# Kernel tuning notes

Measured on AMD Instinct MI355X. Metric: run time of the kernel, lower is better.

## Reference

```python
import jax, jax.numpy as jnp
import numpy as np

N_NODES = 100000
N_EDGES = 1600000
D_IN = 128
D_HID = 64
D_EMB = 64
EDGE_DIM = 2 * D_EMB  # 128
N_CASES = 4
BATCH = 16384
BN_EPS = 1e-5


def gcn_conv(x, src, dst, n, W, b):
    # PyG GCNConv: linear transform, add self-loops, sym-normalized aggregation
    h = x @ W  # [N, out]
    loop = jnp.arange(n, dtype=src.dtype)
    s = jnp.concatenate([src, loop])
    d = jnp.concatenate([dst, loop])
    deg = jax.ops.segment_sum(jnp.ones(s.shape[0], dtype=h.dtype), d, num_segments=n)
    dinv = jnp.where(deg > 0, deg ** -0.5, 0.0)
    norm = dinv[s] * dinv[d]  # [E+N]
    msg = h[s] * norm[:, None]
    return jax.ops.segment_sum(msg, d, num_segments=n) + b


def batchnorm(h, gamma, beta):
    # BatchNorm1d in training mode: biased batch statistics over nodes
    mu = h.mean(0)
    var = jnp.mean((h - mu) ** 2, axis=0)
    return (h - mu) * jax.lax.rsqrt(var + BN_EPS) * gamma + beta


def gcn_net(x, src, dst, n, W1, b1, g, be, W2, b2):
    h = gcn_conv(x, src, dst, n, W1, b1)
    h = jax.nn.relu(batchnorm(h, g, be))
    return gcn_conv(h, src, dst, n, W2, b2)


def setup_inputs() -> dict:
    key = jax.random.key(0)
    ks = jax.random.split(key, 20)
    inp = {
        "x": jax.random.normal(ks[0], (N_NODES, D_IN), dtype=jnp.float32),
        "edge_index": jax.random.randint(ks[1], (2, N_EDGES), 0, N_NODES, dtype=jnp.int32),
        "users_tensor": jax.random.randint(ks[2], (BATCH,), 0, 50000, dtype=jnp.int64) if jax.config.jax_enable_x64 else jax.random.randint(ks[2], (BATCH,), 0, 50000, dtype=jnp.int32),
        "items_tensor": jax.random.randint(ks[3], (BATCH,), 0, N_NODES, dtype=jnp.int32),
    }
    s = 0.05
    # generalized GCN params
    inp["W1g"] = jax.random.normal(ks[4], (D_IN, D_HID), dtype=jnp.float32) * s
    inp["b1g"] = jnp.zeros((D_HID,), jnp.float32)
    inp["g1g"] = jnp.ones((D_HID,), jnp.float32)
    inp["be1g"] = jnp.zeros((D_HID,), jnp.float32)
    inp["W2g"] = jax.random.normal(ks[5], (D_HID, D_EMB), dtype=jnp.float32) * s
    inp["b2g"] = jnp.zeros((D_EMB,), jnp.float32)
    # specific GCN params
    inp["W1s"] = jax.random.normal(ks[6], (D_IN, D_HID), dtype=jnp.float32) * s
    inp["b1s"] = jnp.zeros((D_HID,), jnp.float32)
    inp["g1s"] = jnp.ones((D_HID,), jnp.float32)
    inp["be1s"] = jnp.zeros((D_HID,), jnp.float32)
    inp["W2s"] = jax.random.normal(ks[7], (D_HID, D_EMB), dtype=jnp.float32) * s
    inp["b2s"] = jnp.zeros((D_EMB,), jnp.float32)
    # fusion gate (note: original forward uses hidden1 for BOTH inputs)
    inp["Wf1"] = jax.random.normal(ks[8], (EDGE_DIM, EDGE_DIM), dtype=jnp.float32) * s
    inp["Wsig"] = jax.random.normal(ks[9], (2 * EDGE_DIM, 1), dtype=jnp.float32) * s
    # heads
    inp["Wtc"] = jax.random.normal(ks[10], (EDGE_DIM, N_CASES), dtype=jnp.float32) * s
    inp["btc"] = jnp.zeros((N_CASES,), jnp.float32)
    inp["Wp"] = jax.random.normal(ks[11], (EDGE_DIM, 2), dtype=jnp.float32) * s
    inp["bp"] = jnp.zeros((2,), jnp.float32)
    return inp


def reference(x, edge_index, users_tensor, items_tensor,
              W1g, b1g, g1g, be1g, W2g, b2g,
              W1s, b1s, g1s, be1s, W2s, b2s,
              Wf1, Wsig, Wtc, btc, Wp, bp):
    n = x.shape[0]
    src, dst = edge_index[0], edge_index[1]

    nodes_gen = gcn_net(x, src, dst, n, W1g, b1g, g1g, be1g, W2g, b2g)  # [N, D_EMB]
    nodes_spec = gcn_net(x, src, dst, n, W1s, b1s, g1s, be1s, W2s, b2s)

    gen = jnp.concatenate([nodes_gen[users_tensor], nodes_gen[items_tensor]], axis=1)   # [B, 2E]
    spec = jnp.concatenate([nodes_spec[users_tensor], nodes_spec[items_tensor]], axis=1)

    h1 = jnp.tanh(gen @ Wf1)
    h2 = jnp.tanh(spec @ Wf1)  # original reuses hidden1
    z = jax.nn.sigmoid(jnp.concatenate([h1, h2], axis=1) @ Wsig)  # [B,1]
    fused = z * h1 + (1.0 - z) * h2

    link_output = fused @ Wp + bp
    generalized_output = gen @ Wtc + btc
    return (link_output, generalized_output)
```

## Files before the change

### kernel.cpp

```cpp
#include <hip/hip_runtime.h>
#include <hip/hip_bf16.h>


#define ELL_CAP 64
#define BCAP 8192
#define ACHUNK 5120

typedef __attribute__((ext_vector_type(8))) short short8v;
typedef __attribute__((ext_vector_type(4))) float f32x4;

static __device__ __forceinline__ float wred64(float v) {
#pragma unroll
  for (int m = 32; m; m >>= 1) v += __shfl_xor(v, m, 64);
  return v;
}

static __device__ __forceinline__ unsigned short f2bf(float f) {
  unsigned u = __float_as_uint(f);
  unsigned r = (u + 0x7fffu + ((u >> 16) & 1u)) >> 16;
  return (unsigned short)r;
}
static __device__ __forceinline__ unsigned packbf(float a, float b) {
  return (unsigned)f2bf(a) | ((unsigned)f2bf(b) << 16);
}
static __device__ __forceinline__ float bflo(unsigned u) {
  return __uint_as_float(u << 16);
}
static __device__ __forceinline__ float bfhi(unsigned u) {
  return __uint_as_float(u & 0xffff0000u);
}

__global__ void k_prep(const float* __restrict__ x, unsigned* __restrict__ bff,
                       int* __restrict__ gbump, float* __restrict__ stats,
                       const float* __restrict__ W1g, const float* __restrict__ b1g,
                       const float* __restrict__ W1s, const float* __restrict__ b1s,
                       const float* __restrict__ W2g, const float* __restrict__ b2g,
                       const float* __restrict__ W2s, const float* __restrict__ b2s,
                       const float* __restrict__ Wf1,
                       short* __restrict__ Wb1, short* __restrict__ Wb2,
                       short* __restrict__ WbH, float* __restrict__ bc1,
                       float* __restrict__ bc2, int n, int NB) {
  int idx = blockIdx.x * 256 + threadIdx.x;
  int n16 = n * 16;
  if (idx < n16) {
    const float4* f4 = (const float4*)x;
    float4 a = f4[idx * 2], b = f4[idx * 2 + 1];
    uint4 o;
    o.x = packbf(a.x, a.y);
    o.y = packbf(a.z, a.w);
    o.z = packbf(b.x, b.y);
    o.w = packbf(b.z, b.w);
    ((uint4*)bff)[idx] = o;
  }
  if (idx < 16384) {
    int k = idx >> 7, c = idx & 127;
    int pi = (k >> 3) * 1024 + c * 8 + (k & 7);
    float w1 = (c < 64) ? W1g[k * 64 + c] : W1s[k * 64 + (c - 64)];
    Wb1[pi] = (short)f2bf(w1);
    float w2 = 0.f;
    if (k < 64 && c < 64) w2 = W2g[k * 64 + c];
    else if (k >= 64 && c >= 64) w2 = W2s[(k - 64) * 64 + (c - 64)];
    Wb2[pi] = (short)f2bf(w2);
    WbH[pi] = (short)f2bf(Wf1[k * 128 + c]);
  }
  if (idx < 128) {
    bc1[idx] = (idx < 64) ? b1g[idx] : b1s[idx - 64];
    bc2[idx] = (idx < 64) ? b2g[idx] : b2s[idx - 64];
  }
  if (idx < NB) gbump[idx] = idx * BCAP;
  if (idx < 2048) stats[idx] = 0.f;
}

__global__ __launch_bounds__(256) void k_bucketA(
    const int* __restrict__ src, const int* __restrict__ dst,
    int* __restrict__ gbump, unsigned* __restrict__ ebuf, int E, int NB) {
  __shared__ int hist[512];
  __shared__ int gbase[512];
  int t = threadIdx.x;
  int e0 = blockIdx.x * ACHUNK;
  int m = min(ACHUNK, E - e0);
  for (int b = t; b < NB; b += 256) hist[b] = 0;
  __syncthreads();
  for (int i = t; i < m; i += 256) atomicAdd(&hist[dst[e0 + i] >> 8], 1);
  __syncthreads();
  for (int b = t; b < NB; b += 256) {
    gbase[b] = hist[b] ? atomicAdd(&gbump[b], hist[b]) : 0;
    hist[b] = 0;
  }
  __syncthreads();
  for (int i = t; i < m; i += 256) {
    int d = dst[e0 + i];
    int s = src[e0 + i];
    int b = d >> 8;
    int off = gbase[b] + atomicAdd(&hist[b], 1);
    if (off < (b + 1) * BCAP)
      ebuf[off] = ((unsigned)s << 8) | (unsigned)(d & 255);
  }
}

__global__ __launch_bounds__(256) void k_csrB(
    const unsigned* __restrict__ ebuf, const int* __restrict__ gbump,
    int* __restrict__ cnt, float* __restrict__ dinv, int* __restrict__ col,
    int n) {
  __shared__ int lbump[256];
  int b = blockIdx.x;
  lbump[threadIdx.x] = 0;
  __syncthreads();
  int base = b * BCAP;
  int m = min(gbump[b] - base, BCAP);
  for (int i = threadIdx.x; i < m; i += 256) {
    unsigned p = ebuf[base + i];
    int dloc = p & 255;
    int slot = atomicAdd(&lbump[dloc], 1);
    if (slot < ELL_CAP)
      col[(b * 256 + dloc) * ELL_CAP + slot] = (int)(p >> 8);
  }
  __syncthreads();
  int node = b * 256 + threadIdx.x;
  if (node < n) {
    int c = lbump[threadIdx.x];
    cnt[node] = min(c, ELL_CAP);
    dinv[node] = rsqrtf((float)(c + 1));
  }
}

template <bool BN>
__global__ __launch_bounds__(256) void k_agg(
    const unsigned* __restrict__ featb, unsigned* __restrict__ outb,
    const int* __restrict__ cnt, const float* __restrict__ dinv,
    const int* __restrict__ col,
    const float* __restrict__ stats, const float* __restrict__ g1g,
    const float* __restrict__ be1g, const float* __restrict__ g1s,
    const float* __restrict__ be1s, float inv_n, int n) {
  __shared__ float sc_sh[128], sf_sh[128];
  if (BN) {
    int c = threadIdx.x;
    if (c < 128) {
      float s = 0.f, q = 0.f;
#pragma unroll
      for (int k = 0; k < 8; k++) {
        s += stats[k * 256 + c];
        q += stats[k * 256 + 128 + c];
      }
      float mu = s * inv_n;
      float var = q * inv_n - mu * mu;
      float gam = (c < 64) ? g1g[c] : g1s[c - 64];
      float bet = (c < 64) ? be1g[c] : be1s[c - 64];
      float scv = gam * rsqrtf(var + 1e-5f);
      sc_sh[c] = scv;
      sf_sh[c] = bet - mu * scv;
    }
    __syncthreads();
  }
  int node = blockIdx.x * 16 + (threadIdx.x >> 4);
  if (node >= n) return;
  int t = threadIdx.x & 15;
  float sc[8], sf[8];
  if (BN) {
#pragma unroll
    for (int j = 0; j < 8; j++) {
      sc[j] = sc_sh[8 * t + j];
      sf[j] = sf_sh[8 * t + j];
    }
  }
  const uint4* f4 = (const uint4*)featb;
  float di = dinv[node];
  float acc[8];
  {
    uint4 sv = f4[node * 16 + t];
    float f[8] = {bflo(sv.x), bfhi(sv.x), bflo(sv.y), bfhi(sv.y),
                  bflo(sv.z), bfhi(sv.z), bflo(sv.w), bfhi(sv.w)};
#pragma unroll
    for (int j = 0; j < 8; j++) {
      if (BN) f[j] = fmaxf(f[j] * sc[j] + sf[j], 0.f);
      acc[j] = f[j] * di;
    }
  }
  int m = cnt[node];
  const int4* cl = (const int4*)&col[node * ELL_CAP];
  int i = 0;
  for (; i + 8 <= m; i += 8) {
    int4 c0 = cl[i >> 2];
    int4 c1 = cl[(i >> 2) + 1];
    int ss[8] = {c0.x, c0.y, c0.z, c0.w, c1.x, c1.y, c1.z, c1.w};
    float ww[8];
    uint4 vv[8];
#pragma unroll
    for (int q = 0; q < 8; q++) {
      ww[q] = dinv[ss[q]];
      vv[q] = f4[ss[q] * 16 + t];
    }
#pragma unroll
    for (int q = 0; q < 8; q++) {
      float w = ww[q];
      uint4 v = vv[q];
      float f[8] = {bflo(v.x), bfhi(v.x), bflo(v.y), bfhi(v.y),
                    bflo(v.z), bfhi(v.z), bflo(v.w), bfhi(v.w)};
#pragma unroll
      for (int j = 0; j < 8; j++) {
        if (BN) f[j] = fmaxf(f[j] * sc[j] + sf[j], 0.f);
        acc[j] += f[j] * w;
      }
    }
  }
  for (; i + 4 <= m; i += 4) {
    int4 c4 = cl[i >> 2];
    int ss[4] = {c4.x, c4.y, c4.z, c4.w};
#pragma unroll
    for (int q = 0; q < 4; q++) {
      int s = ss[q];
      float w = dinv[s];
      uint4 v = f4[s * 16 + t];
      float f[8] = {bflo(v.x), bfhi(v.x), bflo(v.y), bfhi(v.y),
                    bflo(v.z), bfhi(v.z), bflo(v.w), bfhi(v.w)};
#pragma unroll
      for (int j = 0; j < 8; j++) {
        if (BN) f[j] = fmaxf(f[j] * sc[j] + sf[j], 0.f);
        acc[j] += f[j] * w;
      }
    }
  }
  for (; i < m; ++i) {
    int s = col[node * ELL_CAP + i];
    float w = dinv[s];
    uint4 v = f4[s * 16 + t];
    float f[8] = {bflo(v.x), bfhi(v.x), bflo(v.y), bfhi(v.y),
                  bflo(v.z), bfhi(v.z), bflo(v.w), bfhi(v.w)};
#pragma unroll
    for (int j = 0; j < 8; j++) {
      if (BN) f[j] = fmaxf(f[j] * sc[j] + sf[j], 0.f);
      acc[j] += f[j] * w;
    }
  }
  uint4 o;
  o.x = packbf(acc[0] * di, acc[1] * di);
  o.y = packbf(acc[2] * di, acc[3] * di);
  o.z = packbf(acc[4] * di, acc[5] * di);
  o.w = packbf(acc[6] * di, acc[7] * di);
  ((uint4*)outb)[node * 16 + t] = o;
}

template <bool CBF16, bool STATS, bool TANH, bool GATHER>
__global__ __launch_bounds__(256) void k_mgemm(
    const unsigned* __restrict__ Abf, const unsigned short* __restrict__ nodesb,
    const int* __restrict__ users, const int* __restrict__ items,
    const short* __restrict__ Wb, const float* __restrict__ bias,
    void* __restrict__ Cvp, int M, float* __restrict__ stats) {
  __shared__ short Wl[16384];
  __shared__ float shs[128], shq[128];
  {
    const uint4* s4 = (const uint4*)Wb;
    uint4* d4 = (uint4*)Wl;
    for (int i = threadIdx.x; i < 2048; i += 256) d4[i] = s4[i];
  }
  if (STATS && threadIdx.x < 128) { shs[threadIdx.x] = 0.f; shq[threadIdx.x] = 0.f; }
  __syncthreads();
  int lane = threadIdx.x & 63;
  int wv = threadIdx.x >> 6;
  int l15 = lane & 15;
  int l4 = lane >> 4;
  int row = blockIdx.x * 64 + wv * 16 + l15;
  int rc = min(row, M - 1);
  bool valid = row < M;

  short8v afr[4];
  if (GATHER) {
    int fo = blockIdx.y * 64;
    const short* pu = (const short*)nodesb + users[rc] * 128 + fo;
    const short* pi = (const short*)nodesb + items[rc] * 128 + fo;
#pragma unroll
    for (int ks = 0; ks < 4; ks++) {
      int k = ks * 32 + l4 * 8;
      const short* p = (ks < 2) ? (pu + k) : (pi + (k - 64));
      afr[ks] = *(const short8v*)p;
    }
  } else {
    const short* Ab = (const short*)Abf + (size_t)rc * 128;
#pragma unroll
    for (int ks = 0; ks < 4; ks++)
      afr[ks] = *(const short8v*)(Ab + ks * 32 + l4 * 8);
  }

  f32x4 acc[8];
#pragma unroll
  for (int nt = 0; nt < 8; nt++) acc[nt] = (f32x4){0.f, 0.f, 0.f, 0.f};
#pragma unroll
  for (int nt = 0; nt < 8; nt++) {
#pragma unroll
    for (int ks = 0; ks < 4; ks++) {
      int kb = ks * 4 + l4;
      short8v w = *(const short8v*)&Wl[kb * 1024 + (nt * 16 + l15) * 8];
      acc[nt] = __builtin_amdgcn_mfma_f32_16x16x32_bf16(w, afr[ks], acc[nt], 0, 0, 0);
    }
  }

#pragma unroll
  for (int nt = 0; nt < 8; nt++) {
    int c0 = nt * 16 + l4 * 4;
    float o[4];
#pragma unroll
    for (int r = 0; r < 4; r++) o[r] = acc[nt][r];
    if (bias) {
      float4 bv = *(const float4*)(bias + c0);
      o[0] += bv.x; o[1] += bv.y; o[2] += bv.z; o[3] += bv.w;
    }
    if (TANH) {
#pragma unroll
      for (int r = 0; r < 4; r++) o[r] = tanhf(o[r]);
    }
    if (STATS) {
      float s[4], q[4];
#pragma unroll
      for (int r = 0; r < 4; r++) {
        s[r] = valid ? o[r] : 0.f;
        q[r] = s[r] * s[r];
      }
#pragma unroll
      for (int m = 1; m < 16; m <<= 1) {
#pragma unroll
        for (int r = 0; r < 4; r++) {
          s[r] += __shfl_xor(s[r], m, 64);
          q[r] += __shfl_xor(q[r], m, 64);
        }
      }
      if (l15 == 0) {
#pragma unroll
        for (int r = 0; r < 4; r++) {
          atomicAdd(&shs[c0 + r], s[r]);
          atomicAdd(&shq[c0 + r], q[r]);
        }
      }
    }
    if (valid) {
      if (CBF16) {
        unsigned* Cb = (unsigned*)Cvp;
        uint2 p;
        p.x = packbf(o[0], o[1]);
        p.y = packbf(o[2], o[3]);
        *(uint2*)&Cb[(size_t)row * 64 + (c0 >> 1)] = p;
      } else {
        float* Cf = (float*)Cvp + (size_t)blockIdx.y * M * 128;
        *(float4*)&Cf[(size_t)row * 128 + c0] = make_float4(o[0], o[1], o[2], o[3]);
      }
    }
  }
  if (STATS) {
    __syncthreads();
    if (threadIdx.x < 128) {
      float* st = stats + (blockIdx.x & 7) * 256;
      atomicAdd(&st[threadIdx.x], shs[threadIdx.x]);
      atomicAdd(&st[128 + threadIdx.x], shq[threadIdx.x]);
    }
  }
}

__global__ void k_head(const float* __restrict__ G1, const float* __restrict__ G2,
                       const unsigned short* __restrict__ nodesb,
                       const int* __restrict__ users,
                       const int* __restrict__ items, const float* __restrict__ Wsig,
                       const float* __restrict__ Wtc, const float* __restrict__ btc,
                       const float* __restrict__ Wp, const float* __restrict__ bp,
                       float* __restrict__ out, int B) {
  int l = threadIdx.x & 63;
  int wave = (blockIdx.x * 256 + threadIdx.x) >> 6;
  int nw = (gridDim.x * 256) >> 6;
  for (int b = wave; b < B; b += nw) {
    const float* g1 = G1 + (size_t)b * 128;
    const float* g2 = G2 + (size_t)b * 128;
    int u = users[b], it = items[b];
    float h1a = g1[l], h1b = g1[64 + l];
    float h2a = g2[l], h2b = g2[64 + l];
    float ga = __uint_as_float((unsigned)nodesb[u * 128 + l] << 16);
    float gb = __uint_as_float((unsigned)nodesb[it * 128 + l] << 16);
    float zp = h1a * Wsig[l] + h1b * Wsig[64 + l] + h2a * Wsig[128 + l] + h2b * Wsig[192 + l];
    float z = wred64(zp);
    z = 1.f / (1.f + expf(-z));
    float fa = z * h1a + (1.f - z) * h2a;
    float fb = z * h1b + (1.f - z) * h2b;
    float p0 = wred64(fa * Wp[l * 2] + fb * Wp[(64 + l) * 2]);
    float p1 = wred64(fa * Wp[l * 2 + 1] + fb * Wp[(64 + l) * 2 + 1]);
    float t0 = wred64(ga * Wtc[l * 4] + gb * Wtc[(64 + l) * 4]);
    float t1 = wred64(ga * Wtc[l * 4 + 1] + gb * Wtc[(64 + l) * 4 + 1]);
    float t2 = wred64(ga * Wtc[l * 4 + 2] + gb * Wtc[(64 + l) * 4 + 2]);
    float t3 = wred64(ga * Wtc[l * 4 + 3] + gb * Wtc[(64 + l) * 4 + 3]);
    if (l == 0) {
      out[b * 2] = p0 + bp[0];
      out[b * 2 + 1] = p1 + bp[1];
      float* go = out + 2 * B;
      go[b * 4] = t0 + btc[0];
      go[b * 4 + 1] = t1 + btc[1];
      go[b * 4 + 2] = t2 + btc[2];
      go[b * 4 + 3] = t3 + btc[3];
    }
  }
}

extern "C" void kernel_launch(void* const* d_in, const int* in_sizes, int n_in,
                              void* d_out, int out_size, void* d_ws, size_t ws_size,
                              hipStream_t stream) {
  const float* x = (const float*)d_in[0];
  const int* ei = (const int*)d_in[1];
  const int* users = (const int*)d_in[2];
  const int* items = (const int*)d_in[3];
  const float* W1g = (const float*)d_in[4];
  const float* b1g = (const float*)d_in[5];
  const float* g1g = (const float*)d_in[6];
  const float* be1g = (const float*)d_in[7];
  const float* W2g = (const float*)d_in[8];
  const float* b2g = (const float*)d_in[9];
  const float* W1s = (const float*)d_in[10];
  const float* b1s = (const float*)d_in[11];
  const float* g1s = (const float*)d_in[12];
  const float* be1s = (const float*)d_in[13];
  const float* W2s = (const float*)d_in[14];
  const float* b2s = (const float*)d_in[15];
  const float* Wf1 = (const float*)d_in[16];
  const float* Wsig = (const float*)d_in[17];
  const float* Wtc = (const float*)d_in[18];
  const float* btc = (const float*)d_in[19];
  const float* Wp = (const float*)d_in[20];
  const float* bp = (const float*)d_in[21];

  int n = in_sizes[0] / 128;
  int E = in_sizes[1] / 2;
  int B = in_sizes[2];
  int NB = (n + 255) >> 8;
  const int* srcp = ei;
  const int* dstp = ei + E;
  float* out = (float*)d_out;

  char* w = (char*)d_ws;
  auto alloc = [&](size_t bytes) -> char* {
    char* p = w;
    w += (bytes + 255) & ~(size_t)255;
    return p;
  };
  unsigned* xab = (unsigned*)alloc((size_t)n * 64 * 4);
  float* big1 = (float*)alloc((size_t)n * 128 * 4);
  unsigned* bff = (unsigned*)alloc((size_t)n * 128 * 2);
  int* col = (int*)alloc((size_t)n * ELL_CAP * 4);
  unsigned* ebuf = (unsigned*)alloc((size_t)NB * BCAP * 4);
  int* cnt = (int*)alloc((size_t)n * 4);
  float* dinv = (float*)alloc((size_t)n * 4);
  int* gbump = (int*)alloc(512 * 4);
  short* Wb1 = (short*)alloc(16384 * 2);
  short* Wb2 = (short*)alloc(16384 * 2);
  short* WbH = (short*)alloc(16384 * 2);
  float* bc1 = (float*)alloc(512);
  float* bc2 = (float*)alloc(512);
  float* stats = (float*)alloc(2048 * 4);

  k_prep<<<(n * 16 + 255) / 256, 256, 0, stream>>>(
      x, bff, gbump, stats, W1g, b1g, W1s, b1s, W2g, b2g, W2s, b2s, Wf1,
      Wb1, Wb2, WbH, bc1, bc2, n, NB);
  k_bucketA<<<(E + ACHUNK - 1) / ACHUNK, 256, 0, stream>>>(srcp, dstp, gbump, ebuf, E, NB);
  k_csrB<<<NB, 256, 0, stream>>>(ebuf, gbump, cnt, dinv, col, n);

  unsigned* hb = (unsigned*)big1;
  unsigned short* nodesb = (unsigned short*)big1;

  k_agg<false><<<(n + 15) / 16, 256, 0, stream>>>(bff, xab, cnt, dinv, col,
                                                  nullptr, nullptr, nullptr,
                                                  nullptr, nullptr, 0.f, n);
  k_mgemm<true, true, false, false><<<(n + 63) / 64, 256, 0, stream>>>(
      xab, nullptr, nullptr, nullptr, Wb1, bc1, hb, n, stats);

  k_agg<true><<<(n + 15) / 16, 256, 0, stream>>>(hb, xab, cnt, dinv, col,
                                                 stats, g1g, be1g, g1s, be1s,
                                                 1.f / (float)n, n);
  k_mgemm<true, false, false, false><<<(n + 63) / 64, 256, 0, stream>>>(
      xab, nullptr, nullptr, nullptr, Wb2, bc2, nodesb, n, nullptr);

  float* G1 = (float*)bff;
  dim3 gh((B + 63) / 64, 2);
  k_mgemm<false, false, true, true><<<gh, 256, 0, stream>>>(
      nullptr, nodesb, users, items, WbH, nullptr, G1, B, nullptr);
  float* G2 = G1 + (size_t)B * 128;
  k_head<<<2048, 256, 0, stream>>>(G1, G2, nodesb, users, items, Wsig, Wtc, btc,
                                   Wp, bp, out, B);
}
```

Before: 275.8 us.

## Fuse head GEMM and link head into one MFMA kernel; drop 8-wide agg unroll

Result: faster. 250.5 us (-9.2%).

```diff
diff --git a/kernel.cpp b/kernel.cpp
--- a/kernel.cpp
+++ b/kernel.cpp
@@ -8,12 +8,6 @@
 
 typedef __attribute__((ext_vector_type(8))) short short8v;
 typedef __attribute__((ext_vector_type(4))) float f32x4;
-
-static __device__ __forceinline__ float wred64(float v) {
-#pragma unroll
-  for (int m = 32; m; m >>= 1) v += __shfl_xor(v, m, 64);
-  return v;
-}
 
 static __device__ __forceinline__ unsigned short f2bf(float f) {
   unsigned u = __float_as_uint(f);
@@ -28,6 +22,9 @@
 }
 static __device__ __forceinline__ float bfhi(unsigned u) {
   return __uint_as_float(u & 0xffff0000u);
+}
+static __device__ __forceinline__ float bf2f(short s) {
+  return __uint_as_float((unsigned)(unsigned short)s << 16);
 }
 
 __global__ void k_prep(const float* __restrict__ x, unsigned* __restrict__ bff,
@@ -179,30 +176,6 @@
   int m = cnt[node];
   const int4* cl = (const int4*)&col[node * ELL_CAP];
   int i = 0;
-  for (; i + 8 <= m; i += 8) {
-    int4 c0 = cl[i >> 2];
-    int4 c1 = cl[(i >> 2) + 1];
-    int ss[8] = {c0.x, c0.y, c0.z, c0.w, c1.x, c1.y, c1.z, c1.w};
-    float ww[8];
-    uint4 vv[8];
-#pragma unroll
-    for (int q = 0; q < 8; q++) {
-      ww[q] = dinv[ss[q]];
-      vv[q] = f4[ss[q] * 16 + t];
-    }
-#pragma unroll
-    for (int q = 0; q < 8; q++) {
-      float w = ww[q];
-      uint4 v = vv[q];
-      float f[8] = {bflo(v.x), bfhi(v.x), bflo(v.y), bfhi(v.y),
-                    bflo(v.z), bfhi(v.z), bflo(v.w), bfhi(v.w)};
-#pragma unroll
-      for (int j = 0; j < 8; j++) {
-        if (BN) f[j] = fmaxf(f[j] * sc[j] + sf[j], 0.f);
-        acc[j] += f[j] * w;
-      }
-    }
-  }
   for (; i + 4 <= m; i += 4) {
     int4 c4 = cl[i >> 2];
     int ss[4] = {c4.x, c4.y, c4.z, c4.w};
@@ -240,10 +213,9 @@
   ((uint4*)outb)[node * 16 + t] = o;
 }
 
-template <bool CBF16, bool STATS, bool TANH, bool GATHER>
+template <bool CBF16, bool STATS>
 __global__ __launch_bounds__(256) void k_mgemm(
-    const unsigned* __restrict__ Abf, const unsigned short* __restrict__ nodesb,
-    const int* __restrict__ users, const int* __restrict__ items,
+    const unsigned* __restrict__ Abf,
     const short* __restrict__ Wb, const float* __restrict__ bias,
     void* __restrict__ Cvp, int M, float* __restrict__ stats) {
   __shared__ short Wl[16384];
@@ -264,22 +236,10 @@
   bool valid = row < M;
 
   short8v afr[4];
-  if (GATHER) {
-    int fo = blockIdx.y * 64;
-    const short* pu = (const short*)nodesb + users[rc] * 128 + fo;
-    const short* pi = (const short*)nodesb + items[rc] * 128 + fo;
-#pragma unroll
-    for (int ks = 0; ks < 4; ks++) {
-      int k = ks * 32 + l4 * 8;
-      const short* p = (ks < 2) ? (pu + k) : (pi + (k - 64));
-      afr[ks] = *(const short8v*)p;
-    }
-  } else {
-    const short* Ab = (const short*)Abf + (size_t)rc * 128;
-#pragma unroll
-    for (int ks = 0; ks < 4; ks++)
-      afr[ks] = *(const short8v*)(Ab + ks * 32 + l4 * 8);
-  }
+  const short* Ab = (const short*)Abf + (size_t)rc * 128;
+#pragma unroll
+  for (int ks = 0; ks < 4; ks++)
+    afr[ks] = *(const short8v*)(Ab + ks * 32 + l4 * 8);
 
   f32x4 acc[8];
 #pragma unroll
@@ -303,10 +263,6 @@
     if (bias) {
       float4 bv = *(const float4*)(bias + c0);
       o[0] += bv.x; o[1] += bv.y; o[2] += bv.z; o[3] += bv.w;
-    }
-    if (TANH) {
-#pragma unroll
-      for (int r = 0; r < 4; r++) o[r] = tanhf(o[r]);
     }
     if (STATS) {
       float s[4], q[4];
@@ -339,7 +295,7 @@
         p.y = packbf(o[2], o[3]);
         *(uint2*)&Cb[(size_t)row * 64 + (c0 >> 1)] = p;
       } else {
-        float* Cf = (float*)Cvp + (size_t)blockIdx.y * M * 128;
+        float* Cf = (float*)Cvp;
         *(float4*)&Cf[(size_t)row * 128 + c0] = make_float4(o[0], o[1], o[2], o[3]);
       }
     }
@@ -354,44 +310,120 @@
   }
 }
 
-__global__ void k_head(const float* __restrict__ G1, const float* __restrict__ G2,
-                       const unsigned short* __restrict__ nodesb,
-                       const int* __restrict__ users,
-                       const int* __restrict__ items, const float* __restrict__ Wsig,
-                       const float* __restrict__ Wtc, const float* __restrict__ btc,
-                       const float* __restrict__ Wp, const float* __restrict__ bp,
-                       float* __restrict__ out, int B) {
-  int l = threadIdx.x & 63;
-  int wave = (blockIdx.x * 256 + threadIdx.x) >> 6;
-  int nw = (gridDim.x * 256) >> 6;
-  for (int b = wave; b < B; b += nw) {
-    const float* g1 = G1 + (size_t)b * 128;
-    const float* g2 = G2 + (size_t)b * 128;
-    int u = users[b], it = items[b];
-    float h1a = g1[l], h1b = g1[64 + l];
-    float h2a = g2[l], h2b = g2[64 + l];
-    float ga = __uint_as_float((unsigned)nodesb[u * 128 + l] << 16);
-    float gb = __uint_as_float((unsigned)nodesb[it * 128 + l] << 16);
-    float zp = h1a * Wsig[l] + h1b * Wsig[64 + l] + h2a * Wsig[128 + l] + h2b * Wsig[192 + l];
-    float z = wred64(zp);
-    z = 1.f / (1.f + expf(-z));
-    float fa = z * h1a + (1.f - z) * h2a;
-    float fb = z * h1b + (1.f - z) * h2b;
-    float p0 = wred64(fa * Wp[l * 2] + fb * Wp[(64 + l) * 2]);
-    float p1 = wred64(fa * Wp[l * 2 + 1] + fb * Wp[(64 + l) * 2 + 1]);
-    float t0 = wred64(ga * Wtc[l * 4] + gb * Wtc[(64 + l) * 4]);
-    float t1 = wred64(ga * Wtc[l * 4 + 1] + gb * Wtc[(64 + l) * 4 + 1]);
-    float t2 = wred64(ga * Wtc[l * 4 + 2] + gb * Wtc[(64 + l) * 4 + 2]);
-    float t3 = wred64(ga * Wtc[l * 4 + 3] + gb * Wtc[(64 + l) * 4 + 3]);
-    if (l == 0) {
-      out[b * 2] = p0 + bp[0];
-      out[b * 2 + 1] = p1 + bp[1];
-      float* go = out + 2 * B;
-      go[b * 4] = t0 + btc[0];
-      go[b * 4 + 1] = t1 + btc[1];
-      go[b * 4 + 2] = t2 + btc[2];
-      go[b * 4 + 3] = t3 + btc[3];
-    }
+__global__ __launch_bounds__(256) void k_fhead(
+    const unsigned short* __restrict__ nodesb,
+    const int* __restrict__ users, const int* __restrict__ items,
+    const short* __restrict__ WbH, const float* __restrict__ Wsig,
+    const float* __restrict__ Wtc, const float* __restrict__ btc,
+    const float* __restrict__ Wp, const float* __restrict__ bp,
+    float* __restrict__ out, int B) {
+  __shared__ short Wl[16384];
+  __shared__ float WsigL[256], WpL[256], WtcL[512];
+  {
+    const uint4* s4 = (const uint4*)WbH;
+    uint4* d4 = (uint4*)Wl;
+    for (int i = threadIdx.x; i < 2048; i += 256) d4[i] = s4[i];
+    if (threadIdx.x < 256) {
+      WsigL[threadIdx.x] = Wsig[threadIdx.x];
+      WpL[threadIdx.x] = Wp[threadIdx.x];
+    }
+    for (int i = threadIdx.x; i < 512; i += 256) WtcL[i] = Wtc[i];
+  }
+  __syncthreads();
+  int lane = threadIdx.x & 63;
+  int wv = threadIdx.x >> 6;
+  int l15 = lane & 15;
+  int l4 = lane >> 4;
+  int row = blockIdx.x * 64 + wv * 16 + l15;
+  int rc = min(row, B - 1);
+  int u = users[rc], it = items[rc];
+  const short* pu = (const short*)nodesb + u * 128;
+  const short* pi = (const short*)nodesb + it * 128;
+
+  short8v ag[4], as[4];
+#pragma unroll
+  for (int ks = 0; ks < 4; ks++) {
+    int k = ks * 32 + l4 * 8;
+    const short* pg = (ks < 2) ? (pu + k) : (pi + (k - 64));
+    const short* ps = (ks < 2) ? (pu + 64 + k) : (pi + k);
+    ag[ks] = *(const short8v*)pg;
+    as[ks] = *(const short8v*)ps;
+  }
+
+  f32x4 a1[8], a2[8];
+#pragma unroll
+  for (int nt = 0; nt < 8; nt++) {
+    a1[nt] = (f32x4){0.f, 0.f, 0.f, 0.f};
+    a2[nt] = (f32x4){0.f, 0.f, 0.f, 0.f};
+  }
+#pragma unroll
+  for (int nt = 0; nt < 8; nt++) {
+#pragma unroll
+    for (int ks = 0; ks < 4; ks++) {
+      int kb = ks * 4 + l4;
+      short8v w = *(const short8v*)&Wl[kb * 1024 + (nt * 16 + l15) * 8];
+      a1[nt] = __builtin_amdgcn_mfma_f32_16x16x32_bf16(w, ag[ks], a1[nt], 0, 0, 0);
+      a2[nt] = __builtin_amdgcn_mfma_f32_16x16x32_bf16(w, as[ks], a2[nt], 0, 0, 0);
+    }
+  }
+
+  float zp = 0.f;
+#pragma unroll
+  for (int nt = 0; nt < 8; nt++) {
+    int c0 = nt * 16 + l4 * 4;
+#pragma unroll
+    for (int r = 0; r < 4; r++) {
+      float h1 = tanhf(a1[nt][r]);
+      float h2 = tanhf(a2[nt][r]);
+      a1[nt][r] = h1;
+      a2[nt][r] = h2;
+      zp += h1 * WsigL[c0 + r] + h2 * WsigL[128 + c0 + r];
+    }
+  }
+  zp += __shfl_xor(zp, 16, 64);
+  zp += __shfl_xor(zp, 32, 64);
+  float z = 1.f / (1.f + expf(-zp));
+
+  float p0 = 0.f, p1 = 0.f;
+#pragma unroll
+  for (int nt = 0; nt < 8; nt++) {
+    int c0 = nt * 16 + l4 * 4;
+#pragma unroll
+    for (int r = 0; r < 4; r++) {
+      float fu = z * a1[nt][r] + (1.f - z) * a2[nt][r];
+      p0 += fu * WpL[(c0 + r) * 2];
+      p1 += fu * WpL[(c0 + r) * 2 + 1];
+    }
+  }
+  float t0 = 0.f, t1 = 0.f, t2 = 0.f, t3 = 0.f;
+#pragma unroll
+  for (int ks = 0; ks < 4; ks++) {
+    int kbase = ks * 32 + l4 * 8;
+#pragma unroll
+    for (int j = 0; j < 8; j++) {
+      float g = bf2f(ag[ks][j]);
+      int c = kbase + j;
+      t0 += g * WtcL[c * 4];
+      t1 += g * WtcL[c * 4 + 1];
+      t2 += g * WtcL[c * 4 + 2];
+      t3 += g * WtcL[c * 4 + 3];
+    }
+  }
+  p0 += __shfl_xor(p0, 16, 64); p0 += __shfl_xor(p0, 32, 64);
+  p1 += __shfl_xor(p1, 16, 64); p1 += __shfl_xor(p1, 32, 64);
+  t0 += __shfl_xor(t0, 16, 64); t0 += __shfl_xor(t0, 32, 64);
+  t1 += __shfl_xor(t1, 16, 64); t1 += __shfl_xor(t1, 32, 64);
+  t2 += __shfl_xor(t2, 16, 64); t2 += __shfl_xor(t2, 32, 64);
+  t3 += __shfl_xor(t3, 16, 64); t3 += __shfl_xor(t3, 32, 64);
+
+  if (l4 == 0 && row < B) {
+    out[row * 2] = p0 + bp[0];
+    out[row * 2 + 1] = p1 + bp[1];
+    float* go = out + 2 * B;
+    go[row * 4] = t0 + btc[0];
+    go[row * 4 + 1] = t1 + btc[1];
+    go[row * 4 + 2] = t2 + btc[2];
+    go[row * 4 + 3] = t3 + btc[3];
   }
 }
 
@@ -462,20 +494,13 @@
   k_agg<false><<<(n + 15) / 16, 256, 0, stream>>>(bff, xab, cnt, dinv, col,
                                                   nullptr, nullptr, nullptr,
                                                   nullptr, nullptr, 0.f, n);
-  k_mgemm<true, true, false, false><<<(n + 63) / 64, 256, 0, stream>>>(
-      xab, nullptr, nullptr, nullptr, Wb1, bc1, hb, n, stats);
+  k_mgemm<true, true><<<(n + 63) / 64, 256, 0, stream>>>(xab, Wb1, bc1, hb, n, stats);
 
   k_agg<true><<<(n + 15) / 16, 256, 0, stream>>>(hb, xab, cnt, dinv, col,
                                                  stats, g1g, be1g, g1s, be1s,
                                                  1.f / (float)n, n);
-  k_mgemm<true, false, false, false><<<(n + 63) / 64, 256, 0, stream>>>(
-      xab, nullptr, nullptr, nullptr, Wb2, bc2, nodesb, n, nullptr);
-
-  float* G1 = (float*)bff;
-  dim3 gh((B + 63) / 64, 2);
-  k_mgemm<false, false, true, true><<<gh, 256, 0, stream>>>(
-      nullptr, nodesb, users, items, WbH, nullptr, G1, B, nullptr);
-  float* G2 = G1 + (size_t)B * 128;
-  k_head<<<2048, 256, 0, stream>>>(G1, G2, nodesb, users, items, Wsig, Wtc, btc,
-                                   Wp, bp, out, B);
-}
+  k_mgemm<true, false><<<(n + 63) / 64, 256, 0, stream>>>(xab, Wb2, bc2, nodesb, n, nullptr);
+
+  k_fhead<<<(B + 63) / 64, 256, 0, stream>>>(nodesb, users, items, WbH, Wsig,
+                                             Wtc, btc, Wp, bp, out, B);
+}
```
